# Kernel optimization log

Hardware: AMD Instinct MI355X
Metric: run time of the kernel (lower is better)

The kernel has to match this reference:

```python
import jax, jax.numpy as jnp
import numpy as np

N = 20000        # nodes
E = 160000       # edges
MUL = 64         # multiplicity per irrep (0e and 1o)
EDIM = 8         # scalar edge-embedding dim (radial basis)
NZ = 4           # node-attr (species one-hot) channels
AVG_NEIGH = 8.0  # avg_num_neighbors
INV_SQRT3 = float(1.0 / np.sqrt(3.0))  # CG norm for 1o x 1o -> 0e


def setup_inputs() -> dict:
    key = jax.random.key(0)
    ks = jax.random.split(key, 13)
    s = lambda fan: 1.0 / np.sqrt(fan)
    return {
        "node_feats": jax.random.normal(ks[0], (N, 256), jnp.float32),          # 64x0e | 64x1o (flattened)
        "node_attrs": jax.random.uniform(ks[1], (N, NZ), jnp.float32),
        "edge_attrs": jax.random.normal(ks[2], (E, 4), jnp.float32),            # SH lmax=1: [Y0 | Y1(3)]
        "edge_embedding": jax.random.normal(ks[3], (E, EDIM), jnp.float32),
        # linear_1 (per-irrep channel mixing)
        "W_lin1_0": jax.random.normal(ks[4], (MUL, MUL), jnp.float32),
        "W_lin1_1": jax.random.normal(ks[5], (MUL, MUL), jnp.float32),
        # radial MLP: EDIM -> EDIM -> 4*MUL tp weights
        "W_mlp1": jax.random.normal(ks[6], (EDIM, EDIM), jnp.float32),
        "W_mlp2": jax.random.normal(ks[7], (EDIM, 4 * MUL), jnp.float32),
        # linear_2: 128x0e+128x1o -> 128x0e+64x1o
        "W_lin2_0": jax.random.normal(ks[8], (2 * MUL, 2 * MUL), jnp.float32),
        "W_lin2_1": jax.random.normal(ks[9], (2 * MUL, MUL), jnp.float32),
        # self-connection FCTP weights: (u, z, w)
        "W_sc0": jax.random.normal(ks[10], (MUL, NZ, 2 * MUL), jnp.float32),
        "W_sc1": jax.random.normal(ks[11], (MUL, NZ, MUL), jnp.float32),
        "edge_index": jax.random.randint(ks[12], (2, E), 0, N, dtype=jnp.int32),
    }


def reference(node_feats, node_attrs, edge_attrs, edge_embedding,
              W_lin1_0, W_lin1_1, W_mlp1, W_mlp2,
              W_lin2_0, W_lin2_1, W_sc0, W_sc1, edge_index):
    edge_src, edge_dst = edge_index[0], edge_index[1]

    # split node feats into irrep blocks: 64x0e scalars, 64x1o vectors
    x0 = node_feats[:, :MUL]                         # [N, 64]
    x1 = node_feats[:, MUL:].reshape(N, MUL, 3)      # [N, 64, 3]

    # linear_1 (e3nn Linear, per-irrep, 1/sqrt(fan_in))
    inv = 1.0 / np.sqrt(MUL)
    h0 = (x0 @ W_lin1_0) * inv                       # [N, 64]
    h1 = jnp.einsum("nud,uv->nvd", x1, W_lin1_1) * inv

    # radial MLP -> per-edge UVU weights (e3nn FullyConnectedNet: no bias, silu, 1/sqrt(fan_in))
    inv_e = 1.0 / np.sqrt(EDIM)
    hid = jax.nn.silu((edge_embedding @ W_mlp1) * inv_e)
    w = (hid @ W_mlp2) * inv_e                       # [E, 4*MUL]
    w1, w2, w3, w4 = w[:, :MUL], w[:, MUL:2*MUL], w[:, 2*MUL:3*MUL], w[:, 3*MUL:]

    # gather source-node features per edge
    g0 = h0[edge_src]                                # [E, 64]
    g1 = h1[edge_src]                                # [E, 64, 3]
    a0 = edge_attrs[:, :1]                           # [E, 1]  Y0
    a1 = edge_attrs[:, 1:]                           # [E, 3]  Y1

    # UVU tensor product paths (v = 1 for SH attrs)
    m0_a = w1 * g0 * a0                              # 0e x 0e -> 0e
    m0_b = w4 * jnp.einsum("eud,ed->eu", g1, a1) * INV_SQRT3   # 1o x 1o -> 0e
    m1_a = (w2 * g0)[:, :, None] * a1[:, None, :]    # 0e x 1o -> 1o
    m1_b = (w3[:, :, None] * g1) * a0[:, :, None]    # 1o x 0e -> 1o
    msg0 = jnp.concatenate([m0_a, m0_b], axis=1)     # [E, 128]
    msg1 = jnp.concatenate([m1_a, m1_b], axis=1)     # [E, 128, 3]

    # scatter_add to destination nodes, normalize by sqrt(avg_num_neighbors)
    inv_n = 1.0 / np.sqrt(AVG_NEIGH)
    s0 = jax.ops.segment_sum(msg0, edge_dst, num_segments=N) * inv_n   # [N, 128]
    s1 = jax.ops.segment_sum(msg1, edge_dst, num_segments=N) * inv_n   # [N, 128, 3]

    # linear_2: 128x0e+128x1o -> 128x0e (64 scalars + 64 gates) + 64x1o
    inv2 = 1.0 / np.sqrt(2 * MUL)
    u0 = (s0 @ W_lin2_0) * inv2                      # [N, 128]
    u1 = jnp.einsum("nud,uw->nwd", s1, W_lin2_1) * inv2   # [N, 64, 3]

    # self-connection FCTP with 0e node attrs (species-conditioned linear)
    inv_sc = 1.0 / np.sqrt(MUL * NZ)
    sc0 = jnp.einsum("nu,nz,uzw->nw", x0, node_attrs, W_sc0) * inv_sc
    sc1 = jnp.einsum("nud,nz,uzw->nwd", x1, node_attrs, W_sc1) * inv_sc
    t0 = u0 + sc0                                    # [N, 128]
    t1 = u1 + sc1                                    # [N, 64, 3]

    # Gate nonlinearity: silu on scalars, silu(gates) * vectors
    scalars = jax.nn.silu(t0[:, :MUL])               # [N, 64]
    gates = jax.nn.silu(t0[:, MUL:])                 # [N, 64]
    vectors = gates[:, :, None] * t1                 # [N, 64, 3]

    out = jnp.concatenate([scalars, vectors.reshape(N, MUL * 3)], axis=1)  # [N, 256]
    # resnet (irreps match input)
    return node_feats + out
```

## Files before the change

### kernel.cpp

```cpp
#include <hip/hip_runtime.h>
#include <hip/hip_bf16.h>
#include <math.h>

#define N 20000
#define E 160000
#define MUL 64
#define EDIM 8
#define NZ 4

#define INV_SQRT_MUL 0.125f
#define INV_E 0.35355339059327373f
#define INV_N 0.35355339059327373f
#define INV2 0.08838834764831845f
#define INV_SC 0.0625f
#define INV_SQRT3 0.5773502691896258f

typedef unsigned short u16;
typedef unsigned int u32;
typedef short bf16x8 __attribute__((ext_vector_type(8)));
typedef float f32x4 __attribute__((ext_vector_type(4)));

__device__ __forceinline__ float silu(float v) {
    return v / (1.0f + __expf(-v));
}
__device__ __forceinline__ u16 f2bf(float f) {
    union { float f; unsigned int u; } v; v.f = f;
    unsigned int r = (v.u + 0x7FFFu + ((v.u >> 16) & 1u)) >> 16;
    return (u16)r;
}
__device__ __forceinline__ float bflo(u32 p) {
    union { unsigned int u; float f; } v; v.u = p << 16; return v.f;
}
__device__ __forceinline__ float bfhi(u32 p) {
    union { unsigned int u; float f; } v; v.u = p & 0xFFFF0000u; return v.f;
}
#define MFMA(a, b, c) __builtin_amdgcn_mfma_f32_16x16x32_bf16(a, b, c, 0, 0, 0)


#define PREP_B  5000
#define WCONV_B 320
#define HID_B   5000
#define LIST_B  625

__global__ __launch_bounds__(256) void k_front(
    const float* __restrict__ x,
    const float* __restrict__ eemb, const int* __restrict__ eidx,
    const float* __restrict__ W20, const float* __restrict__ Wsc0,
    const float* __restrict__ W21, const float* __restrict__ Wsc1,
    const float* __restrict__ W0, const float* __restrict__ W1,
    const float* __restrict__ Wm1,
    u16* __restrict__ A1, u16* __restrict__ x1p,
    u16* __restrict__ Bt1m, u16* __restrict__ Bt1z, u16* __restrict__ Bt2,
    u16* __restrict__ W0b, u16* __restrict__ W1b,
    float* __restrict__ hid, int* __restrict__ head, int2* __restrict__ nl)
{
    const int b = blockIdx.x;
    const int tid = threadIdx.x;
    __shared__ float xr[4][256];

    if (b < PREP_B) {
        const int n0 = b * 4;
        #pragma unroll
        for (int t = 0; t < 4; ++t)
            xr[t][tid] = x[(size_t)(n0 + t) * 256 + tid];
        __syncthreads();
        #pragma unroll
        for (int t = 0; t < 4; ++t) {
            const int n = n0 + t;
            if (tid < 64) {
                A1[(size_t)n * 192 + 128 + tid] = f2bf(xr[t][tid]);
            } else {
                int q = tid - 64;
                int d = q >> 6, uu = q & 63;
                x1p[((size_t)n * 3 + d) * 64 + uu] = f2bf(xr[t][64 + uu * 3 + d]);
            }
        }
    } else if (b < PREP_B + WCONV_B) {
        int i = (b - PREP_B) * 256 + tid;
        if (i < 16384) {
            int w = i >> 7, k = i & 127;
            Bt1m[i] = f2bf(W20[k * 128 + w]);
        } else if (i < 49152) {
            int j = i - 16384;
            int z = j >> 13, r = j & 8191, w = r >> 6, k = r & 63;
            Bt1z[j] = f2bf(Wsc0[(k * 4 + z) * 128 + w] * INV_SC);
        } else if (i < 73728) {
            int j = i - 49152;
            int w = j / 384, k = j % 384;
            float v = (k < 128) ? W21[k * 64 + w] : Wsc1[(k - 128) * 64 + w];
            Bt2[j] = f2bf(v);
        } else if (i < 77824) {
            int j = i - 73728;
            int v = j >> 6, u = j & 63;
            W0b[j] = f2bf(W0[u * 64 + v] * INV_SQRT_MUL);
        } else {
            int j = i - 77824;
            int v = j >> 6, u = j & 63;
            W1b[j] = f2bf(W1[u * 64 + v] * INV_SQRT_MUL);
        }
    } else if (b < PREP_B + WCONV_B + HID_B) {
        int i = (b - PREP_B - WCONV_B) * 256 + tid;
        int e = i >> 3, k = i & 7;
        float s = 0.f;
        #pragma unroll
        for (int j = 0; j < 8; ++j)
            s += eemb[(size_t)e * 8 + j] * Wm1[j * 8 + k];
        hid[i] = silu(s * INV_E);
    } else {
        int e = (b - PREP_B - WCONV_B - HID_B) * 256 + tid;
        if (e < E) {
            int src = eidx[e];
            int dst = eidx[E + e];
            int old = atomicExch(&head[dst], e);
            nl[e] = make_int2(old, src);
        }
    }
}

__global__ __launch_bounds__(256) void k_hgemm(
    const u16* __restrict__ A1, const u16* __restrict__ x1p,
    const u16* __restrict__ W0b, const u16* __restrict__ W1b,
    u16* __restrict__ hc)
{
    const int lane = threadIdx.x & 63;
    const int g = blockIdx.x * 4 + (threadIdx.x >> 6);
    const int quad = lane >> 4, l16 = lane & 15;
    const bool isC1 = (g >= 1250);
    const int row0 = isC1 ? (g - 1250) * 16 : g * 16;
    const u16* Ap = isC1 ? (x1p + (size_t)(row0 + l16) * 64)
                         : (A1 + (size_t)(row0 + l16) * 192 + 128);
    const u16* Bp = isC1 ? W1b : W0b;

    f32x4 acc[4] = {};
    #pragma unroll
    for (int k0 = 0; k0 < 64; k0 += 32) {
        bf16x8 a = *(const bf16x8*)(Ap + k0 + quad * 8);
        #pragma unroll
        for (int ct = 0; ct < 4; ++ct) {
            bf16x8 bb = *(const bf16x8*)(Bp + (size_t)(ct * 16 + l16) * 64 + k0 + quad * 8);
            acc[ct] = MFMA(a, bb, acc[ct]);
        }
    }
    #pragma unroll
    for (int ct = 0; ct < 4; ++ct) {
        #pragma unroll
        for (int r = 0; r < 4; ++r) {
            int row = row0 + quad * 4 + r;
            int vv = ct * 16 + l16;
            if (!isC1) {
                hc[(size_t)row * 256 + vv * 4] = f2bf(acc[ct][r]);
            } else {
                int n = row / 3, d = row - 3 * (row / 3);
                hc[(size_t)n * 256 + vv * 4 + 1 + d] = f2bf(acc[ct][r]);
            }
        }
    }
}

__global__ __launch_bounds__(256) void k_gather(
    const int* __restrict__ head, const int2* __restrict__ nl,
    const float* __restrict__ eattr, const float* __restrict__ hid,
    const u32* __restrict__ hc2, const float* __restrict__ Wm2,
    u16* __restrict__ A1, u16* __restrict__ A2g)
{
    const int lane = threadIdx.x & 63;
    const int n = blockIdx.x * 4 + (threadIdx.x >> 6);

    float wm0[8], wm1[8], wm2r[8], wm3[8];
    #pragma unroll
    for (int k = 0; k < 8; ++k) {
        wm0[k]  = Wm2[k * 256 + lane];
        wm1[k]  = Wm2[k * 256 + 64 + lane];
        wm2r[k] = Wm2[k * 256 + 128 + lane];
        wm3[k]  = Wm2[k * 256 + 192 + lane];
    }

    float acc0a = 0.f, acc0b = 0.f;
    float s1a[3] = {0.f, 0.f, 0.f}, s1b[3] = {0.f, 0.f, 0.f};

    int e0 = head[n];
    if (e0 != -1) {
        int2 v0 = nl[e0];
        float4 ea = ((const float4*)eattr)[e0];
        float4 hA = ((const float4*)hid)[(size_t)e0 * 2];
        float4 hB = ((const float4*)hid)[(size_t)e0 * 2 + 1];
        uint2  hp = ((const uint2*)hc2)[(size_t)v0.y * 64 + lane];
        int e1 = v0.x;
        int2 v1 = make_int2(-1, 0);
        if (e1 != -1) v1 = nl[e1];

        while (true) {
            int e2 = -1;
            int2 v2 = make_int2(-1, 0);
            float4 eaN, hAN, hBN; uint2 hpN;
            if (e1 != -1) {
                e2 = v1.x;
                if (e2 != -1) v2 = nl[e2];
                eaN = ((const float4*)eattr)[e1];
                hAN = ((const float4*)hid)[(size_t)e1 * 2];
                hBN = ((const float4*)hid)[(size_t)e1 * 2 + 1];
                hpN = ((const uint2*)hc2)[(size_t)v1.y * 64 + lane];
            }

            float w1 = hA.x*wm0[0]+hA.y*wm0[1]+hA.z*wm0[2]+hA.w*wm0[3]
                     + hB.x*wm0[4]+hB.y*wm0[5]+hB.z*wm0[6]+hB.w*wm0[7];
            float w2 = hA.x*wm1[0]+hA.y*wm1[1]+hA.z*wm1[2]+hA.w*wm1[3]
                     + hB.x*wm1[4]+hB.y*wm1[5]+hB.z*wm1[6]+hB.w*wm1[7];
            float w3 = hA.x*wm2r[0]+hA.y*wm2r[1]+hA.z*wm2r[2]+hA.w*wm2r[3]
                     + hB.x*wm2r[4]+hB.y*wm2r[5]+hB.z*wm2r[6]+hB.w*wm2r[7];
            float w4 = hA.x*wm3[0]+hA.y*wm3[1]+hA.z*wm3[2]+hA.w*wm3[3]
                     + hB.x*wm3[4]+hB.y*wm3[5]+hB.z*wm3[6]+hB.w*wm3[7];
            const float g0 = bflo(hp.x), g1x = bfhi(hp.x);
            const float g1y = bflo(hp.y), g1z = bfhi(hp.y);
            acc0a += w1 * g0 * ea.x;
            acc0b += w4 * (g1x * ea.y + g1y * ea.z + g1z * ea.w);
            const float wg = w2 * g0, w3a = w3 * ea.x;
            s1a[0] += wg * ea.y;  s1a[1] += wg * ea.z;  s1a[2] += wg * ea.w;
            s1b[0] += w3a * g1x;  s1b[1] += w3a * g1y;  s1b[2] += w3a * g1z;

            if (e1 == -1) break;
            ea = eaN; hA = hAN; hB = hBN; hp = hpN;
            e1 = e2; v1 = v2;
        }
    }

    const float f = INV_E * INV_N * INV2;
    u16* a1p = &A1[(size_t)n * 192];
    a1p[lane]      = f2bf(acc0a * f);
    a1p[64 + lane] = f2bf(acc0b * f * INV_SQRT3);
    #pragma unroll
    for (int d = 0; d < 3; ++d) {
        u16* a2p = &A2g[((size_t)n * 3 + d) * 128];
        a2p[lane]      = f2bf(s1a[d] * f);
        a2p[64 + lane] = f2bf(s1b[d] * f);
    }
}

__global__ __launch_bounds__(512, 8) void k_gemm_fused(
    const u16* __restrict__ A1, const u16* __restrict__ A2g,
    const u16* __restrict__ x1p,
    const u16* __restrict__ Bt1m, const u16* __restrict__ Bt1z,
    const u16* __restrict__ Bt2,
    const float* __restrict__ attrs, const float* __restrict__ x,
    float* __restrict__ out)
{
    const int lane = threadIdx.x & 63;
    const int wave = threadIdx.x >> 6;
    const int quad = lane >> 4, l16 = lane & 15;
    const int n0 = blockIdx.x * 16;
    const float4* at4 = (const float4*)attrs;

    __shared__ float st0[16][132];
    __shared__ float st1[48][68];

    if (wave < 4) {
        const u16* a0p  = A1   + (size_t)(n0 + l16) * 192 + quad * 8;
        const u16* b0p  = Bt1m + (size_t)(wave * 16 + l16) * 128 + quad * 8;
        const u16* b1p  = Bt1m + (size_t)((wave + 4) * 16 + l16) * 128 + quad * 8;
        const u16* bz0p = Bt1z + (size_t)(wave * 16 + l16) * 64 + quad * 8;
        const u16* bz1p = Bt1z + (size_t)((wave + 4) * 16 + l16) * 64 + quad * 8;

        f32x4 m0 = {}, m1 = {};
        f32x4 z0[4] = {}, z1[4] = {};

        #pragma unroll
        for (int kt = 0; kt < 4; ++kt) {
            bf16x8 a0 = *(const bf16x8*)(a0p + kt * 32);
            bf16x8 b0 = *(const bf16x8*)(b0p + kt * 32);
            bf16x8 b1 = *(const bf16x8*)(b1p + kt * 32);
            m0 = MFMA(a0, b0, m0);
            m1 = MFMA(a0, b1, m1);
        }
        #pragma unroll
        for (int kt = 0; kt < 2; ++kt) {
            bf16x8 a0 = *(const bf16x8*)(a0p + 128 + kt * 32);
            #pragma unroll
            for (int z = 0; z < 4; ++z) {
                bf16x8 c0 = *(const bf16x8*)(bz0p + z * 8192 + kt * 32);
                bf16x8 c1 = *(const bf16x8*)(bz1p + z * 8192 + kt * 32);
                z0[z] = MFMA(a0, c0, z0[z]);
                z1[z] = MFMA(a0, c1, z1[z]);
            }
        }

        #pragma unroll
        for (int r = 0; r < 4; ++r) {
            const int r0 = quad * 4 + r;
            const float4 a = at4[n0 + r0];
            st0[r0][wave * 16 + l16] =
                m0[r] + a.x * z0[0][r] + a.y * z0[1][r] + a.z * z0[2][r] + a.w * z0[3][r];
            st0[r0][(wave + 4) * 16 + l16] =
                m1[r] + a.x * z1[0][r] + a.y * z1[1][r] + a.z * z1[2][r] + a.w * z1[3][r];
        }
    } else {
        const int ct = wave - 4;
        const u16* a1p = A2g + (size_t)(3 * n0 + l16) * 128 + quad * 8;
        const u16* b2p = Bt2 + (size_t)(ct * 16 + l16) * 384 + quad * 8;
        const u16* xq0 = x1p + (size_t)(3 * n0 + l16) * 64 + quad * 2;

        float4 atv[3];
        #pragma unroll
        for (int rt = 0; rt < 3; ++rt) {
            const int ro = rt * 16 + l16;
            const int nn = (ro * 21846) >> 16;
            const float4 v = at4[n0 + nn];
            atv[rt].x = v.x * INV_SC; atv[rt].y = v.y * INV_SC;
            atv[rt].z = v.z * INV_SC; atv[rt].w = v.w * INV_SC;
        }

        f32x4 mt[3] = {};

        #pragma unroll
        for (int kt = 0; kt < 4; ++kt) {
            const int ko = kt * 32;
            bf16x8 b2 = *(const bf16x8*)(b2p + ko);
            bf16x8 a1 = *(const bf16x8*)(a1p + ko);
            bf16x8 a2 = *(const bf16x8*)(a1p + 16 * 128 + ko);
            bf16x8 a3 = *(const bf16x8*)(a1p + 32 * 128 + ko);
            mt[0] = MFMA(a1, b2, mt[0]);
            mt[1] = MFMA(a2, b2, mt[1]);
            mt[2] = MFMA(a3, b2, mt[2]);
        }
        #pragma unroll
        for (int kt = 0; kt < 8; ++kt) {
            bf16x8 b2 = *(const bf16x8*)(b2p + 128 + kt * 32);
            #pragma unroll
            for (int rt = 0; rt < 3; ++rt) {
                const u32 xp = *(const u32*)(xq0 + rt * 16 * 64 + kt * 8);
                const float xa = bflo(xp), xb = bfhi(xp);
                bf16x8 af;
                af[0] = (short)f2bf(xa * atv[rt].x); af[1] = (short)f2bf(xa * atv[rt].y);
                af[2] = (short)f2bf(xa * atv[rt].z); af[3] = (short)f2bf(xa * atv[rt].w);
                af[4] = (short)f2bf(xb * atv[rt].x); af[5] = (short)f2bf(xb * atv[rt].y);
                af[6] = (short)f2bf(xb * atv[rt].z); af[7] = (short)f2bf(xb * atv[rt].w);
                mt[rt] = MFMA(af, b2, mt[rt]);
            }
        }

        #pragma unroll
        for (int r = 0; r < 4; ++r) {
            const int r0 = quad * 4 + r;
            st1[r0][ct * 16 + l16]      = mt[0][r];
            st1[16 + r0][ct * 16 + l16] = mt[1][r];
            st1[32 + r0][ct * 16 + l16] = mt[2][r];
        }
    }

    const int c = threadIdx.x & 255;
    const int th = threadIdx.x >> 8;
    float xv[8];
    #pragma unroll
    for (int i = 0; i < 8; ++i)
        xv[i] = x[(size_t)(n0 + i * 2 + th) * 256 + c];

    __syncthreads();

    #pragma unroll
    for (int i = 0; i < 8; ++i) {
        const int t = i * 2 + th;
        float o;
        if (c < 64) {
            o = xv[i] + silu(st0[t][c]);
        } else {
            int r = c - 64;
            int w = (r * 21846) >> 16;
            int d = r - w * 3;
            o = xv[i] + silu(st0[t][64 + w]) * st1[t * 3 + d][w];
        }
        out[(size_t)(n0 + t) * 256 + c] = o;
    }
}

extern "C" void kernel_launch(void* const* d_in, const int* in_sizes, int n_in,
                              void* d_out, int out_size, void* d_ws, size_t ws_size,
                              hipStream_t stream) {
    const float* node_feats = (const float*)d_in[0];
    const float* node_attrs = (const float*)d_in[1];
    const float* edge_attrs = (const float*)d_in[2];
    const float* edge_emb   = (const float*)d_in[3];
    const float* W_lin1_0   = (const float*)d_in[4];
    const float* W_lin1_1   = (const float*)d_in[5];
    const float* W_mlp1     = (const float*)d_in[6];
    const float* W_mlp2     = (const float*)d_in[7];
    const float* W_lin2_0   = (const float*)d_in[8];
    const float* W_lin2_1   = (const float*)d_in[9];
    const float* W_sc0      = (const float*)d_in[10];
    const float* W_sc1      = (const float*)d_in[11];
    const int*   edge_index = (const int*)d_in[12];
    float* out = (float*)d_out;

    char* p = (char*)d_ws;
    float* hid = (float*)p;                 p += (size_t)E * 8 * 4;
    u16* hc    = (u16*)p;                   p += (size_t)N * 256 * 2;
    u16* A1    = (u16*)p;                   p += (size_t)N * 192 * 2;
    u16* A2g   = (u16*)p;                   p += (size_t)N * 3 * 128 * 2;
    u16* x1p   = (u16*)p;                   p += (size_t)N * 3 * 64 * 2;
    u16* Bt1m  = (u16*)p;                   p += 16384 * 2;
    u16* Bt1z  = (u16*)p;                   p += 32768 * 2;
    u16* Bt2   = (u16*)p;                   p += 24576 * 2;
    u16* W0b   = (u16*)p;                   p += 4096 * 2;
    u16* W1b   = (u16*)p;                   p += 4096 * 2;
    int* head  = (int*)p;                   p += N * 4;
    int2* nl   = (int2*)p;                  p += (size_t)E * 8;

    hipMemsetAsync(head, 0xFF, N * sizeof(int), stream);

    k_front<<<PREP_B + WCONV_B + HID_B + LIST_B, 256, 0, stream>>>(
        node_feats, edge_emb, edge_index,
        W_lin2_0, W_sc0, W_lin2_1, W_sc1, W_lin1_0, W_lin1_1, W_mlp1,
        A1, x1p, Bt1m, Bt1z, Bt2, W0b, W1b, hid, head, nl);
    k_hgemm<<<1250, 256, 0, stream>>>(A1, x1p, W0b, W1b, hc);
    k_gather<<<N / 4, 256, 0, stream>>>(head, nl, edge_attrs, hid,
                                        (const u32*)hc, W_mlp2, A1, A2g);
    k_gemm_fused<<<1250, 512, 0, stream>>>(A1, A2g, x1p, Bt1m, Bt1z, Bt2,
                                           node_attrs, node_feats, out);
}
```

Measured before the change: 212.5 us.

## Stage GEMM A-tiles into swizzled LDS via async loads and prefetch B operands

```diff
diff --git a/kernel.cpp b/kernel.cpp
--- a/kernel.cpp
+++ b/kernel.cpp
@@ -35,6 +35,12 @@
     union { unsigned int u; float f; } v; v.u = p & 0xFFFF0000u; return v.f;
 }
 #define MFMA(a, b, c) __builtin_amdgcn_mfma_f32_16x16x32_bf16(a, b, c, 0, 0, 0)
+
+__device__ __forceinline__ void gll16(const u16* g, u16* l) {
+    __builtin_amdgcn_global_load_lds(
+        (const __attribute__((address_space(1))) u32*)g,
+        (__attribute__((address_space(3))) u32*)l, 16, 0, 0);
+}
 
 
 #define PREP_B  5000
@@ -236,7 +242,7 @@
     }
 }
 
-__global__ __launch_bounds__(512, 8) void k_gemm_fused(
+__global__ __launch_bounds__(512, 4) void k_gemm_fused(
     const u16* __restrict__ A1, const u16* __restrict__ A2g,
     const u16* __restrict__ x1p,
     const u16* __restrict__ Bt1m, const u16* __restrict__ Bt1z,
@@ -250,38 +256,121 @@
     const int n0 = blockIdx.x * 16;
     const float4* at4 = (const float4*)attrs;
 
+    __shared__ __align__(16) u16 sA1[16 * 192];
+    __shared__ __align__(16) u16 sA2[48 * 128];
     __shared__ float st0[16][132];
     __shared__ float st1[48][68];
 
+    {
+        const u16* gA1 = A1 + (size_t)n0 * 192;
+        const u16* gA2 = A2g + (size_t)(3 * n0) * 128;
+        #pragma unroll
+        for (int i = 0; i < 3; ++i) {
+            const int cc = wave + i * 8;
+            if (cc < 6) {
+                const int Lu = cc * 512 + lane * 8;
+                const int row = Lu / 192;
+                const int src = Lu ^ ((row & 7) << 3);
+                gll16(gA1 + src, &sA1[cc * 512]);
+            } else if (cc < 18) {
+                const int Lu = (cc - 6) * 512 + lane * 8;
+                const int row = Lu >> 7;
+                const int src = Lu ^ ((row & 7) << 3);
+                gll16(gA2 + src, &sA2[(cc - 6) * 512]);
+            }
+        }
+    }
+
+    const u16 *bz0p = nullptr, *bz1p = nullptr;
+    bf16x8 PB[8], PC[8];
+    u32 XQ[3][8];
+    float4 atv[3];
+
     if (wave < 4) {
-        const u16* a0p  = A1   + (size_t)(n0 + l16) * 192 + quad * 8;
-        const u16* b0p  = Bt1m + (size_t)(wave * 16 + l16) * 128 + quad * 8;
-        const u16* b1p  = Bt1m + (size_t)((wave + 4) * 16 + l16) * 128 + quad * 8;
-        const u16* bz0p = Bt1z + (size_t)(wave * 16 + l16) * 64 + quad * 8;
-        const u16* bz1p = Bt1z + (size_t)((wave + 4) * 16 + l16) * 64 + quad * 8;
-
+        const u16* b0p = Bt1m + (size_t)(wave * 16 + l16) * 128 + quad * 8;
+        const u16* b1p = Bt1m + (size_t)((wave + 4) * 16 + l16) * 128 + quad * 8;
+        bz0p = Bt1z + (size_t)(wave * 16 + l16) * 64 + quad * 8;
+        bz1p = Bt1z + (size_t)((wave + 4) * 16 + l16) * 64 + quad * 8;
+        #pragma unroll
+        for (int kt = 0; kt < 4; ++kt) {
+            PB[kt]     = *(const bf16x8*)(b0p + kt * 32);
+            PB[4 + kt] = *(const bf16x8*)(b1p + kt * 32);
+        }
+        #pragma unroll
+        for (int z = 0; z < 2; ++z)
+            #pragma unroll
+            for (int kt = 0; kt < 2; ++kt) {
+                PC[z * 2 + kt]     = *(const bf16x8*)(bz0p + z * 8192 + kt * 32);
+                PC[4 + z * 2 + kt] = *(const bf16x8*)(bz1p + z * 8192 + kt * 32);
+            }
+    } else {
+        const int ct = wave - 4;
+        const u16* b2p = Bt2 + (size_t)(ct * 16 + l16) * 384 + quad * 8;
+        const u16* xq0 = x1p + (size_t)(3 * n0 + l16) * 64 + quad * 2;
+        #pragma unroll
+        for (int kt = 0; kt < 4; ++kt)
+            PB[kt] = *(const bf16x8*)(b2p + kt * 32);
+        #pragma unroll
+        for (int kt = 0; kt < 8; ++kt) {
+            bf16x8 v = *(const bf16x8*)(b2p + 128 + kt * 32);
+            if (kt < 4) PB[4 + kt] = v; else PC[kt - 4] = v;
+        }
+        #pragma unroll
+        for (int rt = 0; rt < 3; ++rt)
+            #pragma unroll
+            for (int kt = 0; kt < 8; ++kt)
+                XQ[rt][kt] = *(const u32*)(xq0 + rt * 16 * 64 + kt * 8);
+        #pragma unroll
+        for (int rt = 0; rt < 3; ++rt) {
+            const int ro = rt * 16 + l16;
+            const int nn = (ro * 21846) >> 16;
+            const float4 v = at4[n0 + nn];
+            atv[rt].x = v.x * INV_SC; atv[rt].y = v.y * INV_SC;
+            atv[rt].z = v.z * INV_SC; atv[rt].w = v.w * INV_SC;
+        }
+    }
+
+    const int c = threadIdx.x & 255;
+    const int th = threadIdx.x >> 8;
+    float xv[8];
+    #pragma unroll
+    for (int i = 0; i < 8; ++i)
+        xv[i] = x[(size_t)(n0 + i * 2 + th) * 256 + c];
+
+    __syncthreads();
+
+    if (wave < 4) {
         f32x4 m0 = {}, m1 = {};
+        #pragma unroll
+        for (int kt = 0; kt < 4; ++kt) {
+            const int off = l16 * 192 + kt * 32 + quad * 8;
+            bf16x8 a0 = *(const bf16x8*)(sA1 + (off ^ ((l16 & 7) << 3)));
+            m0 = MFMA(a0, PB[kt], m0);
+            m1 = MFMA(a0, PB[4 + kt], m1);
+        }
+        bf16x8 a0s[2];
+        #pragma unroll
+        for (int kt = 0; kt < 2; ++kt) {
+            const int off = l16 * 192 + 128 + kt * 32 + quad * 8;
+            a0s[kt] = *(const bf16x8*)(sA1 + (off ^ ((l16 & 7) << 3)));
+        }
         f32x4 z0[4] = {}, z1[4] = {};
-
-        #pragma unroll
-        for (int kt = 0; kt < 4; ++kt) {
-            bf16x8 a0 = *(const bf16x8*)(a0p + kt * 32);
-            bf16x8 b0 = *(const bf16x8*)(b0p + kt * 32);
-            bf16x8 b1 = *(const bf16x8*)(b1p + kt * 32);
-            m0 = MFMA(a0, b0, m0);
-            m1 = MFMA(a0, b1, m1);
-        }
-        #pragma unroll
-        for (int kt = 0; kt < 2; ++kt) {
-            bf16x8 a0 = *(const bf16x8*)(a0p + 128 + kt * 32);
-            #pragma unroll
-            for (int z = 0; z < 4; ++z) {
-                bf16x8 c0 = *(const bf16x8*)(bz0p + z * 8192 + kt * 32);
-                bf16x8 c1 = *(const bf16x8*)(bz1p + z * 8192 + kt * 32);
-                z0[z] = MFMA(a0, c0, z0[z]);
-                z1[z] = MFMA(a0, c1, z1[z]);
-            }
-        }
+        #pragma unroll
+        for (int z = 0; z < 2; ++z)
+            #pragma unroll
+            for (int kt = 0; kt < 2; ++kt) {
+                z0[z] = MFMA(a0s[kt], PC[z * 2 + kt], z0[z]);
+                z1[z] = MFMA(a0s[kt], PC[4 + z * 2 + kt], z1[z]);
+            }
+        #pragma unroll
+        for (int z = 0; z < 2; ++z)
+            #pragma unroll
+            for (int kt = 0; kt < 2; ++kt) {
+                bf16x8 d0 = *(const bf16x8*)(bz0p + (z + 2) * 8192 + kt * 32);
+                bf16x8 d1 = *(const bf16x8*)(bz1p + (z + 2) * 8192 + kt * 32);
+                z0[z + 2] = MFMA(a0s[kt], d0, z0[z + 2]);
+                z1[z + 2] = MFMA(a0s[kt], d1, z1[z + 2]);
+            }
 
         #pragma unroll
         for (int r = 0; r < 4; ++r) {
@@ -294,39 +383,23 @@
         }
     } else {
         const int ct = wave - 4;
-        const u16* a1p = A2g + (size_t)(3 * n0 + l16) * 128 + quad * 8;
-        const u16* b2p = Bt2 + (size_t)(ct * 16 + l16) * 384 + quad * 8;
-        const u16* xq0 = x1p + (size_t)(3 * n0 + l16) * 64 + quad * 2;
-
-        float4 atv[3];
-        #pragma unroll
-        for (int rt = 0; rt < 3; ++rt) {
-            const int ro = rt * 16 + l16;
-            const int nn = (ro * 21846) >> 16;
-            const float4 v = at4[n0 + nn];
-            atv[rt].x = v.x * INV_SC; atv[rt].y = v.y * INV_SC;
-            atv[rt].z = v.z * INV_SC; atv[rt].w = v.w * INV_SC;
-        }
-
         f32x4 mt[3] = {};
-
         #pragma unroll
         for (int kt = 0; kt < 4; ++kt) {
-            const int ko = kt * 32;
-            bf16x8 b2 = *(const bf16x8*)(b2p + ko);
-            bf16x8 a1 = *(const bf16x8*)(a1p + ko);
-            bf16x8 a2 = *(const bf16x8*)(a1p + 16 * 128 + ko);
-            bf16x8 a3 = *(const bf16x8*)(a1p + 32 * 128 + ko);
-            mt[0] = MFMA(a1, b2, mt[0]);
-            mt[1] = MFMA(a2, b2, mt[1]);
-            mt[2] = MFMA(a3, b2, mt[2]);
+            #pragma unroll
+            for (int rt = 0; rt < 3; ++rt) {
+                const int row = rt * 16 + l16;
+                const int off = row * 128 + kt * 32 + quad * 8;
+                bf16x8 a = *(const bf16x8*)(sA2 + (off ^ ((row & 7) << 3)));
+                mt[rt] = MFMA(a, PB[kt], mt[rt]);
+            }
         }
         #pragma unroll
         for (int kt = 0; kt < 8; ++kt) {
-            bf16x8 b2 = *(const bf16x8*)(b2p + 128 + kt * 32);
+            const bf16x8 b2 = (kt < 4) ? PB[4 + kt] : PC[kt - 4];
             #pragma unroll
             for (int rt = 0; rt < 3; ++rt) {
-                const u32 xp = *(const u32*)(xq0 + rt * 16 * 64 + kt * 8);
+                const u32 xp = XQ[rt][kt];
                 const float xa = bflo(xp), xb = bfhi(xp);
                 bf16x8 af;
                 af[0] = (short)f2bf(xa * atv[rt].x); af[1] = (short)f2bf(xa * atv[rt].y);
@@ -345,13 +418,6 @@
             st1[32 + r0][ct * 16 + l16] = mt[2][r];
         }
     }
-
-    const int c = threadIdx.x & 255;
-    const int th = threadIdx.x >> 8;
-    float xv[8];
-    #pragma unroll
-    for (int i = 0; i < 8; ++i)
-        xv[i] = x[(size_t)(n0 + i * 2 + th) * 256 + c];
 
     __syncthreads();
 
```

New measurement: 205.4 us. -3.3%, faster.
